# Performance work log

Hardware: AMD Instinct MI355X
Metric: run time of the kernel (lower is better)

Reference implementation:

```python
import jax, jax.numpy as jnp
import numpy as np

B, LC, LE, H, V = 128, 256, 257, 512, 128
PAD = 0  # padding_token_index


def lstm_cell(x, h, c, Wih, Whh, b):
    # torch LSTMCell gate order: i, f, g, o
    g = x @ Wih.T + h @ Whh.T + b
    i, f, gg, o = jnp.split(g, 4, axis=-1)
    c = jax.nn.sigmoid(f) * c + jax.nn.sigmoid(i) * jnp.tanh(gg)
    h = jax.nn.sigmoid(o) * jnp.tanh(c)
    return h, c


def setup_inputs() -> dict:
    key = jax.random.key(0)
    ks = jax.random.split(key, 32)
    p = lambda k, shape: jax.random.normal(k, shape, jnp.float32) * 0.05
    d = {
        'C_idx': jax.random.randint(ks[0], (B, LC), 0, V, dtype=jnp.int32),
        'E_idx': jax.random.randint(ks[1], (B, LE), 0, V, dtype=jnp.int32),
        'C_pad': jnp.zeros((B, LC), dtype=bool),
        'enc_Wih_f': p(ks[2], (4 * H, V)),
        'enc_Whh_f': p(ks[3], (4 * H, H)),
        'enc_b_f': p(ks[4], (4 * H,)),
        'enc_Wih_b': p(ks[5], (4 * H, V)),
        'enc_Whh_b': p(ks[6], (4 * H, H)),
        'enc_b_b': p(ks[7], (4 * H,)),
        'dec_Wih': p(ks[8], (4 * H, H + V)),
        'dec_Whh': p(ks[9], (4 * H, H)),
        'dec_b': p(ks[10], (4 * H,)),
        'Wh': p(ks[11], (H, 2 * H)),
        'Wc': p(ks[12], (H, 2 * H)),
        'Wattn': p(ks[13], (H, 2 * H)),
        'Wout': p(ks[14], (H, 3 * H)),
        'Wvocab': p(ks[15], (V, H)),
        'pg_ctx': p(ks[16], (2 * H,)),
        'pg_in': p(ks[17], (V + H,)),
        'pg_h': p(ks[18], (H,)),
        'pg_c': p(ks[19], (H,)),
        'pg_b': p(ks[20], (1,)),
    }
    return d


def _forward(C_idx, E_idx, C_pad, enc_Wih_f, enc_Whh_f, enc_b_f, enc_Wih_b, enc_Whh_b, enc_b_b,
             dec_Wih, dec_Whh, dec_b, Wh, Wc, Wattn, Wout, Wvocab,
             pg_ctx, pg_in, pg_h, pg_c, pg_b):
    C = jax.nn.one_hot(C_idx, V, dtype=jnp.float32)      # [B,LC,V]
    E_emb = jax.nn.one_hot(E_idx, V, dtype=jnp.float32)  # [B,LE,V]
    z = jnp.zeros((B, H), jnp.float32)

    xs = jnp.swapaxes(C, 0, 1)  # [LC,B,V]

    def enc_fwd(carry, x):
        h, c = lstm_cell(x, carry[0], carry[1], enc_Wih_f, enc_Whh_f, enc_b_f)
        return (h, c), h

    def enc_bwd(carry, x):
        h, c = lstm_cell(x, carry[0], carry[1], enc_Wih_b, enc_Whh_b, enc_b_b)
        return (h, c), h

    (hf, cf), Hf = jax.lax.scan(enc_fwd, (z, z), xs)
    (hb, cb), Hb = jax.lax.scan(enc_bwd, (z, z), xs[::-1])
    Hb = Hb[::-1]
    enc = jnp.swapaxes(jnp.concatenate([Hf, Hb], axis=-1), 0, 1)  # [B,LC,2H]

    # decoder init state from final encoder states (fwd;bwd concat)
    h0 = jnp.concatenate([hf, hb], axis=-1) @ Wh.T
    c0 = jnp.concatenate([cf, cb], axis=-1) @ Wc.T

    enc_proj = enc @ Wattn.T  # [B,LC,H]

    def step(carry, x_emb):
        h, c, prev_out = carry
        nin = jnp.concatenate([x_emb, prev_out], axis=1)  # [B,V+H]
        h, c = lstm_cell(nin, h, c, dec_Wih, dec_Whh, dec_b)
        scores = jnp.einsum('blh,bh->bl', enc_proj, h)
        scores = jnp.where(C_pad, -jnp.inf, scores)
        attn = jax.nn.softmax(scores, axis=1)             # [B,LC]
        ctx = jnp.einsum('bl,blh->bh', attn, enc)         # [B,2H]
        t_out = jnp.tanh(jnp.concatenate([h, ctx], axis=1) @ Wout.T)  # [B,H]
        gen = jax.nn.softmax(t_out @ Wvocab.T, axis=1)    # [B,V]
        p_gen = jax.nn.sigmoid(ctx @ pg_ctx + nin @ pg_in + h @ pg_h + c @ pg_c + pg_b[0])[:, None]
        copy_p = attn * (1.0 - p_gen)
        out = jax.vmap(lambda o, idx, a: o.at[idx].add(a))(gen * p_gen, C_idx, copy_p)
        return (h, c, t_out), out

    xs2 = jnp.swapaxes(E_emb[:, :LE - 1], 0, 1)  # teacher inputs, step 0 = start token
    _, preds = jax.lax.scan(step, (h0, c0, z), xs2)
    preds = jnp.swapaxes(preds, 0, 1)  # [B,LE-1,V]

    tgt = E_idx[:, 1:]
    nll = -jnp.take_along_axis(jnp.log(preds), tgt[..., None], axis=2)[..., 0]
    return jnp.where(tgt == PAD, 0.0, nll)  # [B,LE-1], reduction='none'


def reference(C_idx, E_idx, C_pad, enc_Wih_f, enc_Whh_f, enc_b_f, enc_Wih_b, enc_Whh_b, enc_b_b,
              dec_Wih, dec_Whh, dec_b, Wh, Wc, Wattn, Wout, Wvocab,
              pg_ctx, pg_in, pg_h, pg_c, pg_b):
    return _forward(C_idx, E_idx, C_pad, enc_Wih_f, enc_Whh_f, enc_b_f, enc_Wih_b, enc_Whh_b, enc_b_b,
                    dec_Wih, dec_Whh, dec_b, Wh, Wc, Wattn, Wout, Wvocab,
                    pg_ctx, pg_in, pg_h, pg_c, pg_b)
```

## Files before the change

### kernel.cpp

```cpp
#include <hip/hip_runtime.h>

static constexpr int B_   = 128;
static constexpr int LC_  = 256;
static constexpr int LE_  = 257;
static constexpr int H_   = 512;
static constexpr size_t HB_ = (size_t)512 * 128;

static constexpr size_t OFF_ENC    = 0;
static constexpr size_t SZ_ENC     = (size_t)128 * 256 * 1024 * 2;
static constexpr size_t OFF_WIHFT  = OFF_ENC + SZ_ENC;
static constexpr size_t OFF_WIHBT  = OFF_WIHFT + (size_t)128 * 2048 * 4;
static constexpr size_t OFF_XDEC   = OFF_WIHBT + (size_t)128 * 2048 * 4;
static constexpr size_t OFF_WATTNT = OFF_XDEC + (size_t)128 * 2048 * 4;
static constexpr size_t OFF_HENC   = OFF_WATTNT + (size_t)1024 * 512 * 4;
static constexpr size_t OFF_CENC   = OFF_HENC + 4 * HB_ * 4;
static constexpr size_t OFF_HDEC   = OFF_CENC + 2 * HB_ * 4;
static constexpr size_t OFF_CDEC   = OFF_HDEC + 2 * HB_ * 4;
static constexpr size_t OFF_TOUT   = OFF_CDEC + HB_ * 4;
static constexpr size_t OFF_U      = OFF_TOUT + 2 * HB_ * 4;
static constexpr size_t OFF_CTX    = OFF_U + (size_t)1024 * 128 * 4;
static constexpr size_t OFF_SC     = OFF_CTX + (size_t)1024 * 128 * 4;
static constexpr size_t OFF_MD     = OFF_SC + (size_t)128 * 256 * 4;

__device__ __forceinline__ float sigm(float x) { return 1.f / (1.f + expf(-x)); }
__device__ __forceinline__ unsigned short f2bf(float f) {
  unsigned u = __float_as_uint(f);
  u += 0x7fffu + ((u >> 16) & 1u);
  return (unsigned short)(u >> 16);
}
__device__ __forceinline__ float bfl(unsigned w) { return __uint_as_float(w << 16); }
__device__ __forceinline__ float bfh(unsigned w) { return __uint_as_float(w & 0xffff0000u); }

__global__ __launch_bounds__(256) void k_pre(const float* __restrict__ wihF,
                                             const float* __restrict__ wihB,
                                             const float* __restrict__ dWih,
                                             const float* __restrict__ Wattn,
                                             float* __restrict__ ws) {
  float* WT_F = (float*)((char*)ws + OFF_WIHFT);
  float* WT_B = (float*)((char*)ws + OFF_WIHBT);
  float* XD   = (float*)((char*)ws + OFF_XDEC);
  float* WAT  = (float*)((char*)ws + OFF_WATTNT);
  int stride = gridDim.x * blockDim.x;
  int i0 = blockIdx.x * blockDim.x + threadIdx.x;
  for (int x = i0; x < 128 * 2048; x += stride) {
    int v = x >> 11, n = x & 2047;
    WT_F[x] = wihF[n * 128 + v];
    WT_B[x] = wihB[n * 128 + v];
    XD[x]   = dWih[n * 640 + v];
  }
  for (int x = i0; x < 1024 * 512; x += stride) {
    int j = x >> 9, i2 = x & 511;
    WAT[x] = Wattn[i2 * 1024 + j];
  }
}

__global__ __launch_bounds__(512) void k_enc(const float* __restrict__ WhhF,
                                             const float* __restrict__ WhhB,
                                             const float* __restrict__ bF,
                                             const float* __restrict__ bB,
                                             const int* __restrict__ C_idx,
                                             float* __restrict__ ws, int t) {
  int p = blockIdx.x * 512 + threadIdx.x;
  int b = p & 127;
  int j = (p >> 7) & 511;
  int dir = p >> 16;
  int jj = __builtin_amdgcn_readfirstlane(j);
  int dd = __builtin_amdgcn_readfirstlane(dir);
  const float* Whh  = dd ? WhhB : WhhF;
  const float* bias = dd ? bB : bF;
  const float* WihT = (const float*)((char*)ws + (dd ? OFF_WIHBT : OFF_WIHFT));
  int l = dd ? (LC_ - 1 - t) : t;
  int cidx = C_idx[b * LC_ + l];
  int par = t & 1;
  const float* hp = (const float*)((char*)ws + OFF_HENC) + (size_t)(dir * 2 + (par ^ 1)) * HB_ + b;

  const float* w0 = Whh + (size_t)jj * 512;
  const float* w1 = Whh + (size_t)(512 + jj) * 512;
  const float* w2 = Whh + (size_t)(1024 + jj) * 512;
  const float* w3 = Whh + (size_t)(1536 + jj) * 512;
  float a0 = bias[jj]        + WihT[(size_t)cidx * 2048 + jj];
  float a1 = bias[512 + jj]  + WihT[(size_t)cidx * 2048 + 512 + jj];
  float a2 = bias[1024 + jj] + WihT[(size_t)cidx * 2048 + 1024 + jj];
  float a3 = bias[1536 + jj] + WihT[(size_t)cidx * 2048 + 1536 + jj];
  for (int k = 0; k < 512; k += 4) {
    float4 W0 = *(const float4*)(w0 + k);
    float4 W1 = *(const float4*)(w1 + k);
    float4 W2 = *(const float4*)(w2 + k);
    float4 W3 = *(const float4*)(w3 + k);
    float h0 = hp[(size_t)k * 128], h1 = hp[(size_t)(k + 1) * 128];
    float h2 = hp[(size_t)(k + 2) * 128], h3 = hp[(size_t)(k + 3) * 128];
    a0 += W0.x * h0 + W0.y * h1 + W0.z * h2 + W0.w * h3;
    a1 += W1.x * h0 + W1.y * h1 + W1.z * h2 + W1.w * h3;
    a2 += W2.x * h0 + W2.y * h1 + W2.z * h2 + W2.w * h3;
    a3 += W3.x * h0 + W3.y * h1 + W3.z * h2 + W3.w * h3;
  }
  float ig = sigm(a0), fg = sigm(a1), gg = tanhf(a2), og = sigm(a3);
  float* cp = (float*)((char*)ws + OFF_CENC) + (size_t)dir * HB_ + (size_t)j * 128 + b;
  float c = fg * (*cp) + ig * gg;
  *cp = c;
  float h = og * tanhf(c);
  ((float*)((char*)ws + OFF_HENC))[(size_t)(dir * 2 + par) * HB_ + (size_t)j * 128 + b] = h;
  ((unsigned short*)((char*)ws + OFF_ENC))[((size_t)b * LC_ + l) * 1024 + dir * 512 + j] = f2bf(h);
}

__global__ __launch_bounds__(512) void k_h0c0(const float* __restrict__ Wh,
                                              const float* __restrict__ Wc,
                                              float* __restrict__ ws) {
  int p = blockIdx.x * 512 + threadIdx.x;
  int b = p & 127;
  int n = (p >> 7) & 511;
  int sel = p >> 16;
  int nn = __builtin_amdgcn_readfirstlane(n);
  int ss = __builtin_amdgcn_readfirstlane(sel);
  const float* W = (ss ? Wc : Wh) + (size_t)nn * 1024;
  const float* hf = (const float*)((char*)ws + OFF_HENC) + (size_t)1 * HB_ + b;
  const float* hb = (const float*)((char*)ws + OFF_HENC) + (size_t)3 * HB_ + b;
  float acc = 0.f;
  for (int k = 0; k < 512; k += 4) {
    float4 Wa = *(const float4*)(W + k);
    float4 Wb = *(const float4*)(W + 512 + k);
    acc += Wa.x * hf[(size_t)k * 128] + Wa.y * hf[(size_t)(k + 1) * 128]
         + Wa.z * hf[(size_t)(k + 2) * 128] + Wa.w * hf[(size_t)(k + 3) * 128];
    acc += Wb.x * hb[(size_t)k * 128] + Wb.y * hb[(size_t)(k + 1) * 128]
         + Wb.z * hb[(size_t)(k + 2) * 128] + Wb.w * hb[(size_t)(k + 3) * 128];
  }
  float* dst = (float*)((char*)ws + (ss ? OFF_CDEC : OFF_HDEC));
  dst[(size_t)n * 128 + b] = acc;
}

__device__ void s4_body(float* __restrict__ ws, float* __restrict__ out,
                        const float* __restrict__ Wvocab, const int* __restrict__ E_idx,
                        const int* __restrict__ C_idx, int b, int t) {
  __shared__ float to[516];
  __shared__ float lgp[128][4];
  __shared__ float lg[128];
  __shared__ float red2[8];
  __shared__ float mx_s[2];
  int tau = threadIdx.x;
  const float* TO = (const float*)((char*)ws + OFF_TOUT) + (size_t)(t & 1) * HB_;
  to[tau + (tau >> 7)] = TO[(size_t)tau * 128 + b];
  __syncthreads();
  int v = tau >> 2, seg = tau & 3;
  const float* wv = Wvocab + (size_t)v * 512 + seg * 128;
  const float* tp = &to[seg * 128 + seg];
  float part = 0.f;
#pragma unroll 8
  for (int i = 0; i < 128; ++i) part += tp[i] * wv[i];
  lgp[v][seg] = part;
  __syncthreads();
  if (tau < 128) lg[tau] = lgp[tau][0] + lgp[tau][1] + lgp[tau][2] + lgp[tau][3];
  __syncthreads();
  if (tau < 64) {
    float m2 = fmaxf(lg[tau], lg[tau + 64]);
    for (int o = 32; o; o >>= 1) m2 = fmaxf(m2, __shfl_xor(m2, o));
    float e = expf(lg[tau] - m2) + expf(lg[tau + 64] - m2);
    for (int o = 32; o; o >>= 1) e += __shfl_xor(e, o);
    if (tau == 0) { mx_s[0] = m2; mx_s[1] = e; }
  }
  const float* MD = (const float*)((char*)ws + OFF_MD);
  float Mb = MD[b], Db = MD[128 + b], pg = MD[256 + b];
  int tgt = E_idx[b * LE_ + t];
  float cm = 0.f;
  if (tau < 256) {
    float s = ((const float*)((char*)ws + OFF_SC))[b * 256 + tau];
    if (C_idx[b * 256 + tau] == tgt) cm = expf(s - Mb);
  }
  for (int o = 32; o; o >>= 1) cm += __shfl_xor(cm, o);
  if ((tau & 63) == 0) red2[tau >> 6] = cm;
  __syncthreads();
  if (tau == 0) {
    float mass = (red2[0] + red2[1] + red2[2] + red2[3]) / Db;
    float gen_tgt = expf(lg[tgt] - mx_s[0]) / mx_s[1];
    float prob = pg * gen_tgt + (1.f - pg) * mass;
    out[b * 256 + (t - 1)] = (tgt == 0) ? 0.f : -logf(prob);
  }
}

__global__ __launch_bounds__(512) void k_dgates(const float* __restrict__ dWih,
                                                const float* __restrict__ dWhh,
                                                const float* __restrict__ db,
                                                const float* __restrict__ Wvocab,
                                                const int* __restrict__ E_idx,
                                                const int* __restrict__ C_idx,
                                                float* __restrict__ ws,
                                                float* __restrict__ out, int t) {
  int tau = threadIdx.x;
  if (blockIdx.x >= 256) {
    if (t > 0) s4_body(ws, out, Wvocab, E_idx, C_idx, blockIdx.x - 256, t);
    return;
  }
  __shared__ float part[4][256];
  int kh = tau >> 8, q = tau & 255;
  int pp = blockIdx.x * 256 + q;
  int b = pp & 127, j = pp >> 7;
  int jj = __builtin_amdgcn_readfirstlane(j);
  int pr = t & 1;
  float a0 = 0.f, a1 = 0.f, a2 = 0.f, a3 = 0.f;
  if (kh == 0) {
    const float* w0 = dWih + (size_t)jj * 640 + 128;
    const float* w1 = dWih + (size_t)(512 + jj) * 640 + 128;
    const float* w2 = dWih + (size_t)(1024 + jj) * 640 + 128;
    const float* w3 = dWih + (size_t)(1536 + jj) * 640 + 128;
    const float* po = (const float*)((char*)ws + OFF_TOUT) + (size_t)pr * HB_ + b;
    for (int k = 0; k < 512; k += 4) {
      float4 W0 = *(const float4*)(w0 + k);
      float4 W1 = *(const float4*)(w1 + k);
      float4 W2 = *(const float4*)(w2 + k);
      float4 W3 = *(const float4*)(w3 + k);
      float h0 = po[(size_t)k * 128], h1 = po[(size_t)(k + 1) * 128];
      float h2 = po[(size_t)(k + 2) * 128], h3 = po[(size_t)(k + 3) * 128];
      a0 += W0.x * h0 + W0.y * h1 + W0.z * h2 + W0.w * h3;
      a1 += W1.x * h0 + W1.y * h1 + W1.z * h2 + W1.w * h3;
      a2 += W2.x * h0 + W2.y * h1 + W2.z * h2 + W2.w * h3;
      a3 += W3.x * h0 + W3.y * h1 + W3.z * h2 + W3.w * h3;
    }
  } else {
    const float* w0 = dWhh + (size_t)jj * 512;
    const float* w1 = dWhh + (size_t)(512 + jj) * 512;
    const float* w2 = dWhh + (size_t)(1024 + jj) * 512;
    const float* w3 = dWhh + (size_t)(1536 + jj) * 512;
    const float* hp = (const float*)((char*)ws + OFF_HDEC) + (size_t)pr * HB_ + b;
    for (int k = 0; k < 512; k += 4) {
      float4 W0 = *(const float4*)(w0 + k);
      float4 W1 = *(const float4*)(w1 + k);
      float4 W2 = *(const float4*)(w2 + k);
      float4 W3 = *(const float4*)(w3 + k);
      float h0 = hp[(size_t)k * 128], h1 = hp[(size_t)(k + 1) * 128];
      float h2 = hp[(size_t)(k + 2) * 128], h3 = hp[(size_t)(k + 3) * 128];
      a0 += W0.x * h0 + W0.y * h1 + W0.z * h2 + W0.w * h3;
      a1 += W1.x * h0 + W1.y * h1 + W1.z * h2 + W1.w * h3;
      a2 += W2.x * h0 + W2.y * h1 + W2.z * h2 + W2.w * h3;
      a3 += W3.x * h0 + W3.y * h1 + W3.z * h2 + W3.w * h3;
    }
    part[0][q] = a0; part[1][q] = a1; part[2][q] = a2; part[3][q] = a3;
  }
  __syncthreads();
  if (kh == 0) {
    int xid = E_idx[b * LE_ + t];
    const float* xg = (const float*)((char*)ws + OFF_XDEC) + (size_t)xid * 2048;
    float g0 = a0 + part[0][q] + db[jj]        + xg[jj];
    float g1 = a1 + part[1][q] + db[512 + jj]  + xg[512 + jj];
    float g2 = a2 + part[2][q] + db[1024 + jj] + xg[1024 + jj];
    float g3 = a3 + part[3][q] + db[1536 + jj] + xg[1536 + jj];
    float ig = sigm(g0), fg = sigm(g1), gg = tanhf(g2), og = sigm(g3);
    float* cp = (float*)((char*)ws + OFF_CDEC) + (size_t)j * 128 + b;
    float c = fg * (*cp) + ig * gg;
    *cp = c;
    ((float*)((char*)ws + OFF_HDEC))[(size_t)(pr ^ 1) * HB_ + (size_t)j * 128 + b] = og * tanhf(c);
  }
}

__global__ __launch_bounds__(512) void k_u(const float* __restrict__ unused,
                                           float* __restrict__ ws, int t) {
  int p = blockIdx.x * 512 + threadIdx.x;
  int b = p & 127, j = p >> 7;
  int jj = __builtin_amdgcn_readfirstlane(j);
  const float* w = (const float*)((char*)ws + OFF_WATTNT) + (size_t)jj * 512;
  const float* hp = (const float*)((char*)ws + OFF_HDEC) + (size_t)((t & 1) ^ 1) * HB_ + b;
  float acc = 0.f;
  for (int k = 0; k < 512; k += 4) {
    float4 W = *(const float4*)(w + k);
    acc += W.x * hp[(size_t)k * 128] + W.y * hp[(size_t)(k + 1) * 128]
         + W.z * hp[(size_t)(k + 2) * 128] + W.w * hp[(size_t)(k + 3) * 128];
  }
  ((float*)((char*)ws + OFF_U))[(size_t)j * 128 + b] = acc;
}

__global__ __launch_bounds__(512) void k_attn(const float* __restrict__ pg_ctx,
                                              const float* __restrict__ pg_in,
                                              const float* __restrict__ pg_h,
                                              const float* __restrict__ pg_c,
                                              const float* __restrict__ pg_b,
                                              const int* __restrict__ E_idx,
                                              const unsigned char* __restrict__ C_pad,
                                              float* __restrict__ ws, int t) {
  __shared__ unsigned short tile[65536];
  __shared__ float u_lds[1032];
  __shared__ float scp[64][9];
  __shared__ float p_lds[64];
  __shared__ float sred[8];
  __shared__ float bc[2];
  int b = blockIdx.x, tau = threadIdx.x;
  int pr = t & 1;
  const float* U = (const float*)((char*)ws + OFF_U);
  u_lds[tau + (tau >> 7)] = U[(size_t)tau * 128 + b];
  {
    int x2 = tau + 512;
    u_lds[x2 + (x2 >> 7)] = U[(size_t)x2 * 128 + b];
  }
  float M = -3.0e38f, D = 0.f, c0 = 0.f, c1 = 0.f;
  const uint4* encb = (const uint4*)((char*)ws + OFF_ENC + (size_t)b * LC_ * 1024 * 2);
  float* SC = (float*)((char*)ws + OFF_SC);
  int l = tau >> 3, seg = tau & 7;
  for (int lb = 0; lb < 4; ++lb) {
    const uint4* src = encb + (size_t)lb * 64 * 128;
#pragma unroll
    for (int it = 0; it < 16; ++it) {
      int fl = it * 512 + tau;
      int r = fl >> 7, cb = fl & 127;
      ((uint4*)tile)[(r << 7) + (cb ^ (r & 7))] = src[fl];
    }
    __syncthreads();
    float acc = 0.f;
#pragma unroll
    for (int ibv = 0; ibv < 16; ++ibv) {
      int blk = (seg * 16 + ibv) ^ (l & 7);
      const uint4 wv = *(const uint4*)&tile[(l << 10) + (blk << 3)];
      const float* up = &u_lds[seg * 128 + ibv * 8 + seg];
      acc += bfl(wv.x) * up[0] + bfh(wv.x) * up[1];
      acc += bfl(wv.y) * up[2] + bfh(wv.y) * up[3];
      acc += bfl(wv.z) * up[4] + bfh(wv.z) * up[5];
      acc += bfl(wv.w) * up[6] + bfh(wv.w) * up[7];
    }
    scp[l][seg] = acc;
    __syncthreads();
    if (tau < 64) {
      float s = scp[tau][0] + scp[tau][1] + scp[tau][2] + scp[tau][3]
              + scp[tau][4] + scp[tau][5] + scp[tau][6] + scp[tau][7];
      int gl = lb * 64 + tau;
      if (C_pad[b * LC_ + gl]) s = -3.0e38f;
      SC[b * 256 + gl] = s;
      float m = s;
      for (int o = 32; o; o >>= 1) m = fmaxf(m, __shfl_xor(m, o));
      float Mn = fmaxf(M, m);
      float pv = expf(s - Mn);
      p_lds[tau] = pv;
      float ds = pv;
      for (int o = 32; o; o >>= 1) ds += __shfl_xor(ds, o);
      if (tau == 0) { bc[0] = m; bc[1] = ds; }
    }
    __syncthreads();
    float Mn = fmaxf(M, bc[0]);
    float scale = expf(M - Mn);
    D = D * scale + bc[1];
    c0 *= scale; c1 *= scale;
    M = Mn;
    {
      int cb0 = tau >> 3, e0 = tau & 7;
      int cb1 = (tau + 512) >> 3;
#pragma unroll 8
      for (int l2 = 0; l2 < 64; ++l2) {
        float pv = p_lds[l2];
        float v0 = bfl((unsigned)tile[(l2 << 10) + (((cb0 ^ (l2 & 7)) << 3) | e0)]);
        float v1 = bfl((unsigned)tile[(l2 << 10) + (((cb1 ^ (l2 & 7)) << 3) | e0)]);
        c0 += pv * v0; c1 += pv * v1;
      }
    }
    __syncthreads();
  }
  float inv = 1.f / D;
  float x0 = c0 * inv, x1 = c1 * inv;
  float* CTX = (float*)((char*)ws + OFF_CTX);
  CTX[(size_t)tau * 128 + b] = x0;
  CTX[(size_t)(tau + 512) * 128 + b] = x1;
  float pp = x0 * pg_ctx[tau] + x1 * pg_ctx[tau + 512];
  pp += ((const float*)((char*)ws + OFF_HDEC))[(size_t)(pr ^ 1) * HB_ + (size_t)tau * 128 + b] * pg_h[tau];
  pp += ((const float*)((char*)ws + OFF_CDEC))[(size_t)tau * 128 + b] * pg_c[tau];
  pp += ((const float*)((char*)ws + OFF_TOUT))[(size_t)pr * HB_ + (size_t)tau * 128 + b] * pg_in[128 + tau];
  for (int o = 32; o; o >>= 1) pp += __shfl_xor(pp, o);
  if ((tau & 63) == 0) sred[tau >> 6] = pp;
  __syncthreads();
  if (tau == 0) {
    float s = sred[0] + sred[1] + sred[2] + sred[3] + sred[4] + sred[5] + sred[6] + sred[7];
    int xid = E_idx[b * LE_ + t];
    s += pg_in[xid] + pg_b[0];
    float* MD = (float*)((char*)ws + OFF_MD);
    MD[256 + b] = sigm(s);
    MD[b] = M;
    MD[128 + b] = D;
  }
}

__global__ __launch_bounds__(512) void k_wout(const float* __restrict__ Wout,
                                              float* __restrict__ ws, int t) {
  __shared__ float part[256];
  int tau = threadIdx.x;
  int kh = tau >> 8, q = tau & 255;
  int pp = blockIdx.x * 256 + q;
  int b = pp & 127, n = pp >> 7;
  int nn = __builtin_amdgcn_readfirstlane(n);
  int pr = t & 1;
  float acc = 0.f;
  if (kh == 0) {
    const float* w = Wout + (size_t)nn * 1536;
    const float* hp = (const float*)((char*)ws + OFF_HDEC) + (size_t)(pr ^ 1) * HB_ + b;
    for (int k = 0; k < 512; k += 4) {
      float4 W = *(const float4*)(w + k);
      acc += W.x * hp[(size_t)k * 128] + W.y * hp[(size_t)(k + 1) * 128]
           + W.z * hp[(size_t)(k + 2) * 128] + W.w * hp[(size_t)(k + 3) * 128];
    }
  } else {
    const float* w = Wout + (size_t)nn * 1536 + 512;
    const float* cp = (const float*)((char*)ws + OFF_CTX) + b;
    for (int k = 0; k < 1024; k += 4) {
      float4 W = *(const float4*)(w + k);
      acc += W.x * cp[(size_t)k * 128] + W.y * cp[(size_t)(k + 1) * 128]
           + W.z * cp[(size_t)(k + 2) * 128] + W.w * cp[(size_t)(k + 3) * 128];
    }
    part[q] = acc;
  }
  __syncthreads();
  if (kh == 0) {
    float s = acc + part[q];
    ((float*)((char*)ws + OFF_TOUT))[(size_t)(pr ^ 1) * HB_ + (size_t)n * 128 + b] = tanhf(s);
  }
}

__global__ __launch_bounds__(512) void k_final(const float* __restrict__ Wvocab,
                                               const int* __restrict__ E_idx,
                                               const int* __restrict__ C_idx,
                                               float* __restrict__ ws,
                                               float* __restrict__ out) {
  s4_body(ws, out, Wvocab, E_idx, C_idx, blockIdx.x, 256);
}

extern "C" void kernel_launch(void* const* d_in, const int* in_sizes, int n_in,
                              void* d_out, int out_size, void* d_ws, size_t ws_size,
                              hipStream_t stream) {
  (void)in_sizes; (void)n_in; (void)out_size; (void)ws_size;
  const int* C_idx = (const int*)d_in[0];
  const int* E_idx = (const int*)d_in[1];
  const unsigned char* C_pad = (const unsigned char*)d_in[2];
  const float* eWihF = (const float*)d_in[3];
  const float* eWhhF = (const float*)d_in[4];
  const float* ebF   = (const float*)d_in[5];
  const float* eWihB = (const float*)d_in[6];
  const float* eWhhB = (const float*)d_in[7];
  const float* ebB   = (const float*)d_in[8];
  const float* dWih  = (const float*)d_in[9];
  const float* dWhh  = (const float*)d_in[10];
  const float* db    = (const float*)d_in[11];
  const float* Wh    = (const float*)d_in[12];
  const float* Wc    = (const float*)d_in[13];
  const float* Wattn = (const float*)d_in[14];
  const float* Wout  = (const float*)d_in[15];
  const float* Wvoc  = (const float*)d_in[16];
  const float* pgc   = (const float*)d_in[17];
  const float* pgi   = (const float*)d_in[18];
  const float* pgh   = (const float*)d_in[19];
  const float* pgcc  = (const float*)d_in[20];
  const float* pgb   = (const float*)d_in[21];
  float* ws = (float*)d_ws;
  float* out = (float*)d_out;

  hipMemsetAsync((char*)d_ws + OFF_HENC, 0, 6 * HB_ * 4, stream);
  hipMemsetAsync((char*)d_ws + OFF_TOUT, 0, 2 * HB_ * 4, stream);

  k_pre<<<512, 256, 0, stream>>>(eWihF, eWihB, dWih, Wattn, ws);
  for (int t = 0; t < 256; ++t)
    k_enc<<<256, 512, 0, stream>>>(eWhhF, eWhhB, ebF, ebB, C_idx, ws, t);
  k_h0c0<<<256, 512, 0, stream>>>(Wh, Wc, ws);
  for (int t = 0; t < 256; ++t) {
    k_dgates<<<384, 512, 0, stream>>>(dWih, dWhh, db, Wvoc, E_idx, C_idx, ws, out, t);
    k_u<<<256, 512, 0, stream>>>(nullptr, ws, t);
    k_attn<<<128, 512, 0, stream>>>(pgc, pgi, pgh, pgcc, pgb, E_idx, C_pad, ws, t);
    k_wout<<<256, 512, 0, stream>>>(Wout, ws, t);
  }
  k_final<<<128, 512, 0, stream>>>(Wvoc, E_idx, C_idx, ws, out);
}
```

Measured before the change: 34.11 ms.

## Replace per-timestep kernel launches with persistent per-batch encoder and decoder kernels

```diff
diff --git a/kernel.cpp b/kernel.cpp
--- a/kernel.cpp
+++ b/kernel.cpp
@@ -1,26 +1,9 @@
 #include <hip/hip_runtime.h>
 
-static constexpr int B_   = 128;
-static constexpr int LC_  = 256;
-static constexpr int LE_  = 257;
-static constexpr int H_   = 512;
-static constexpr size_t HB_ = (size_t)512 * 128;
-
-static constexpr size_t OFF_ENC    = 0;
-static constexpr size_t SZ_ENC     = (size_t)128 * 256 * 1024 * 2;
-static constexpr size_t OFF_WIHFT  = OFF_ENC + SZ_ENC;
-static constexpr size_t OFF_WIHBT  = OFF_WIHFT + (size_t)128 * 2048 * 4;
-static constexpr size_t OFF_XDEC   = OFF_WIHBT + (size_t)128 * 2048 * 4;
-static constexpr size_t OFF_WATTNT = OFF_XDEC + (size_t)128 * 2048 * 4;
-static constexpr size_t OFF_HENC   = OFF_WATTNT + (size_t)1024 * 512 * 4;
-static constexpr size_t OFF_CENC   = OFF_HENC + 4 * HB_ * 4;
-static constexpr size_t OFF_HDEC   = OFF_CENC + 2 * HB_ * 4;
-static constexpr size_t OFF_CDEC   = OFF_HDEC + 2 * HB_ * 4;
-static constexpr size_t OFF_TOUT   = OFF_CDEC + HB_ * 4;
-static constexpr size_t OFF_U      = OFF_TOUT + 2 * HB_ * 4;
-static constexpr size_t OFF_CTX    = OFF_U + (size_t)1024 * 128 * 4;
-static constexpr size_t OFF_SC     = OFF_CTX + (size_t)1024 * 128 * 4;
-static constexpr size_t OFF_MD     = OFF_SC + (size_t)128 * 256 * 4;
+static constexpr size_t OFF_ENC  = 0;
+static constexpr size_t OFF_HFIN = 67108864;
+static constexpr size_t OFF_CFIN = 67633152;
+static constexpr size_t OFF_OVL  = 68157440;
 
 __device__ __forceinline__ float sigm(float x) { return 1.f / (1.f + expf(-x)); }
 __device__ __forceinline__ unsigned short f2bf(float f) {
@@ -30,388 +13,391 @@
 }
 __device__ __forceinline__ float bfl(unsigned w) { return __uint_as_float(w << 16); }
 __device__ __forceinline__ float bfh(unsigned w) { return __uint_as_float(w & 0xffff0000u); }
-
-__global__ __launch_bounds__(256) void k_pre(const float* __restrict__ wihF,
-                                             const float* __restrict__ wihB,
-                                             const float* __restrict__ dWih,
-                                             const float* __restrict__ Wattn,
-                                             float* __restrict__ ws) {
-  float* WT_F = (float*)((char*)ws + OFF_WIHFT);
-  float* WT_B = (float*)((char*)ws + OFF_WIHBT);
-  float* XD   = (float*)((char*)ws + OFF_XDEC);
-  float* WAT  = (float*)((char*)ws + OFF_WATTNT);
-  int stride = gridDim.x * blockDim.x;
-  int i0 = blockIdx.x * blockDim.x + threadIdx.x;
-  for (int x = i0; x < 128 * 2048; x += stride) {
-    int v = x >> 11, n = x & 2047;
-    WT_F[x] = wihF[n * 128 + v];
-    WT_B[x] = wihB[n * 128 + v];
-    XD[x]   = dWih[n * 640 + v];
-  }
-  for (int x = i0; x < 1024 * 512; x += stride) {
-    int j = x >> 9, i2 = x & 511;
-    WAT[x] = Wattn[i2 * 1024 + j];
-  }
-}
-
-__global__ __launch_bounds__(512) void k_enc(const float* __restrict__ WhhF,
-                                             const float* __restrict__ WhhB,
-                                             const float* __restrict__ bF,
+__device__ __forceinline__ float bf2f(unsigned short v) { return __uint_as_float(((unsigned)v) << 16); }
+
+#if defined(__has_builtin)
+#if __has_builtin(__builtin_amdgcn_fdot2_f32_bf16)
+#define HAVE_DOT2BF 1
+#endif
+#endif
+
+#ifdef HAVE_DOT2BF
+typedef __bf16 bf2_t __attribute__((ext_vector_type(2)));
+__device__ __forceinline__ float dot2bf(unsigned w, unsigned h, float acc) {
+  return __builtin_amdgcn_fdot2_f32_bf16(__builtin_bit_cast(bf2_t, w),
+                                         __builtin_bit_cast(bf2_t, h), acc, false);
+}
+#else
+__device__ __forceinline__ float dot2bf(unsigned w, unsigned h, float acc) {
+  return acc + bfl(w) * bfl(h) + bfh(w) * bfh(h);
+}
+#endif
+
+__global__ __launch_bounds__(256) void k_pre1(const float* __restrict__ WhhF,
+                                              const float* __restrict__ WhhB,
+                                              const float* __restrict__ WihF,
+                                              const float* __restrict__ WihB,
+                                              char* __restrict__ wsb) {
+  unsigned short* dst = (unsigned short*)(wsb + OFF_OVL);
+  int id = blockIdx.x * 256 + threadIdx.x;
+  int str = gridDim.x * 256;
+  for (int x = id; x < 2097152; x += str) {
+    int dir = x >> 20, r = x & 1048575;
+    int e = r & 7, j = (r >> 3) & 511, k2 = r >> 12;
+    int g = e >> 1, k = k2 * 2 + (e & 1);
+    const float* W = dir ? WhhB : WhhF;
+    dst[x] = f2bf(W[((size_t)g * 512 + j) * 512 + k]);
+  }
+  for (int x = id; x < 524288; x += str) {
+    int dir = x >> 18, r = x & 262143;
+    int g = r & 3, j = (r >> 2) & 511, v = r >> 11;
+    const float* W = dir ? WihB : WihF;
+    dst[2097152 + x] = f2bf(W[((size_t)g * 512 + j) * 128 + v]);
+  }
+}
+
+__global__ __launch_bounds__(256) void k_pre2(const float* __restrict__ dWih,
+                                              const float* __restrict__ dWhh,
+                                              const float* __restrict__ Wattn,
+                                              const float* __restrict__ Wout,
+                                              const float* __restrict__ Wvoc,
+                                              char* __restrict__ wsb) {
+  unsigned short* dst = (unsigned short*)(wsb + OFF_OVL);
+  int id = blockIdx.x * 256 + threadIdx.x;
+  int str = gridDim.x * 256;
+  for (int x = id; x < 1048576; x += str) {
+    int e = x & 7, j = (x >> 3) & 511, k2 = x >> 12;
+    int g = e >> 1, k = k2 * 2 + (e & 1);
+    dst[x] = f2bf(dWih[((size_t)g * 512 + j) * 640 + 128 + k]);
+  }
+  for (int x = id; x < 1048576; x += str) {
+    int e = x & 7, j = (x >> 3) & 511, k2 = x >> 12;
+    int g = e >> 1, k = k2 * 2 + (e & 1);
+    dst[1048576 + x] = f2bf(dWhh[((size_t)g * 512 + j) * 512 + k]);
+  }
+  for (int x = id; x < 524288; x += str) {
+    int e = x & 3, o = (x >> 2) & 1023, i4 = x >> 12;
+    int i = i4 * 4 + e;
+    dst[2097152 + x] = f2bf(Wattn[(size_t)i * 1024 + o]);
+  }
+  for (int x = id; x < 786432; x += str) {
+    int e = x & 3, j = (x >> 2) & 511, i4 = x >> 11;
+    int i = i4 * 4 + e;
+    dst[2621440 + x] = f2bf(Wout[(size_t)j * 1536 + i]);
+  }
+  for (int x = id; x < 65536; x += str) {
+    int e = x & 3, v = (x >> 2) & 127, i4 = x >> 9;
+    int i = i4 * 4 + e;
+    dst[3407872 + x] = f2bf(Wvoc[(size_t)v * 512 + i]);
+  }
+  for (int x = id; x < 262144; x += str) {
+    int g = x & 3, j = (x >> 2) & 511, v = x >> 11;
+    dst[3473408 + x] = f2bf(dWih[((size_t)g * 512 + j) * 640 + v]);
+  }
+}
+
+__global__ __launch_bounds__(512) void k_enc(const float* __restrict__ bF,
                                              const float* __restrict__ bB,
                                              const int* __restrict__ C_idx,
-                                             float* __restrict__ ws, int t) {
-  int p = blockIdx.x * 512 + threadIdx.x;
-  int b = p & 127;
-  int j = (p >> 7) & 511;
-  int dir = p >> 16;
-  int jj = __builtin_amdgcn_readfirstlane(j);
-  int dd = __builtin_amdgcn_readfirstlane(dir);
-  const float* Whh  = dd ? WhhB : WhhF;
-  const float* bias = dd ? bB : bF;
-  const float* WihT = (const float*)((char*)ws + (dd ? OFF_WIHBT : OFF_WIHFT));
-  int l = dd ? (LC_ - 1 - t) : t;
-  int cidx = C_idx[b * LC_ + l];
-  int par = t & 1;
-  const float* hp = (const float*)((char*)ws + OFF_HENC) + (size_t)(dir * 2 + (par ^ 1)) * HB_ + b;
-
-  const float* w0 = Whh + (size_t)jj * 512;
-  const float* w1 = Whh + (size_t)(512 + jj) * 512;
-  const float* w2 = Whh + (size_t)(1024 + jj) * 512;
-  const float* w3 = Whh + (size_t)(1536 + jj) * 512;
-  float a0 = bias[jj]        + WihT[(size_t)cidx * 2048 + jj];
-  float a1 = bias[512 + jj]  + WihT[(size_t)cidx * 2048 + 512 + jj];
-  float a2 = bias[1024 + jj] + WihT[(size_t)cidx * 2048 + 1024 + jj];
-  float a3 = bias[1536 + jj] + WihT[(size_t)cidx * 2048 + 1536 + jj];
-  for (int k = 0; k < 512; k += 4) {
-    float4 W0 = *(const float4*)(w0 + k);
-    float4 W1 = *(const float4*)(w1 + k);
-    float4 W2 = *(const float4*)(w2 + k);
-    float4 W3 = *(const float4*)(w3 + k);
-    float h0 = hp[(size_t)k * 128], h1 = hp[(size_t)(k + 1) * 128];
-    float h2 = hp[(size_t)(k + 2) * 128], h3 = hp[(size_t)(k + 3) * 128];
-    a0 += W0.x * h0 + W0.y * h1 + W0.z * h2 + W0.w * h3;
-    a1 += W1.x * h0 + W1.y * h1 + W1.z * h2 + W1.w * h3;
-    a2 += W2.x * h0 + W2.y * h1 + W2.z * h2 + W2.w * h3;
-    a3 += W3.x * h0 + W3.y * h1 + W3.z * h2 + W3.w * h3;
-  }
-  float ig = sigm(a0), fg = sigm(a1), gg = tanhf(a2), og = sigm(a3);
-  float* cp = (float*)((char*)ws + OFF_CENC) + (size_t)dir * HB_ + (size_t)j * 128 + b;
-  float c = fg * (*cp) + ig * gg;
-  *cp = c;
-  float h = og * tanhf(c);
-  ((float*)((char*)ws + OFF_HENC))[(size_t)(dir * 2 + par) * HB_ + (size_t)j * 128 + b] = h;
-  ((unsigned short*)((char*)ws + OFF_ENC))[((size_t)b * LC_ + l) * 1024 + dir * 512 + j] = f2bf(h);
-}
-
-__global__ __launch_bounds__(512) void k_h0c0(const float* __restrict__ Wh,
-                                              const float* __restrict__ Wc,
-                                              float* __restrict__ ws) {
-  int p = blockIdx.x * 512 + threadIdx.x;
-  int b = p & 127;
-  int n = (p >> 7) & 511;
-  int sel = p >> 16;
-  int nn = __builtin_amdgcn_readfirstlane(n);
-  int ss = __builtin_amdgcn_readfirstlane(sel);
-  const float* W = (ss ? Wc : Wh) + (size_t)nn * 1024;
-  const float* hf = (const float*)((char*)ws + OFF_HENC) + (size_t)1 * HB_ + b;
-  const float* hb = (const float*)((char*)ws + OFF_HENC) + (size_t)3 * HB_ + b;
-  float acc = 0.f;
-  for (int k = 0; k < 512; k += 4) {
-    float4 Wa = *(const float4*)(W + k);
-    float4 Wb = *(const float4*)(W + 512 + k);
-    acc += Wa.x * hf[(size_t)k * 128] + Wa.y * hf[(size_t)(k + 1) * 128]
-         + Wa.z * hf[(size_t)(k + 2) * 128] + Wa.w * hf[(size_t)(k + 3) * 128];
-    acc += Wb.x * hb[(size_t)k * 128] + Wb.y * hb[(size_t)(k + 1) * 128]
-         + Wb.z * hb[(size_t)(k + 2) * 128] + Wb.w * hb[(size_t)(k + 3) * 128];
-  }
-  float* dst = (float*)((char*)ws + (ss ? OFF_CDEC : OFF_HDEC));
-  dst[(size_t)n * 128 + b] = acc;
-}
-
-__device__ void s4_body(float* __restrict__ ws, float* __restrict__ out,
-                        const float* __restrict__ Wvocab, const int* __restrict__ E_idx,
-                        const int* __restrict__ C_idx, int b, int t) {
-  __shared__ float to[516];
-  __shared__ float lgp[128][4];
-  __shared__ float lg[128];
-  __shared__ float red2[8];
-  __shared__ float mx_s[2];
+                                             char* __restrict__ wsb) {
+  __shared__ __align__(16) unsigned short hbf[512];
+  int bid = blockIdx.x;
+  int b = bid & 127, dir = bid >> 7;
+  int j = threadIdx.x;
+  const unsigned short* WH = (const unsigned short*)(wsb + OFF_OVL) + (size_t)dir * 1048576;
+  const unsigned short* WX = (const unsigned short*)(wsb + OFF_OVL) + 2097152 + (size_t)dir * 262144;
+  const float* bias = dir ? bB : bF;
+  float b0 = bias[j], b1 = bias[512 + j], b2 = bias[1024 + j], b3 = bias[1536 + j];
+  unsigned short* encb = (unsigned short*)wsb + (size_t)b * 262144;
+  const uint4* wp = (const uint4*)WH + j;
+  float c = 0.f, h = 0.f;
+  hbf[j] = 0;
+  __syncthreads();
+  for (int t = 0; t < 256; ++t) {
+    int l = dir ? (255 - t) : t;
+    int cidx = C_idx[b * 256 + l];
+    uint2 xg = *(const uint2*)(WX + ((size_t)cidx * 512 + j) * 4);
+    float a0 = b0 + bfl(xg.x), a1 = b1 + bfh(xg.x);
+    float a2 = b2 + bfl(xg.y), a3 = b3 + bfh(xg.y);
+    for (int k2 = 0; k2 < 256; ++k2) {
+      uint4 w = wp[(size_t)k2 * 512];
+      unsigned hp = *(const unsigned*)((const char*)hbf + k2 * 4);
+      a0 = dot2bf(w.x, hp, a0);
+      a1 = dot2bf(w.y, hp, a1);
+      a2 = dot2bf(w.z, hp, a2);
+      a3 = dot2bf(w.w, hp, a3);
+    }
+    float ig = sigm(a0), fg = sigm(a1), gg = tanhf(a2), og = sigm(a3);
+    c = fg * c + ig * gg;
+    h = og * tanhf(c);
+    __syncthreads();
+    unsigned short hb = f2bf(h);
+    hbf[j] = hb;
+    encb[(size_t)l * 1024 + dir * 512 + j] = hb;
+    __syncthreads();
+  }
+  ((float*)(wsb + OFF_HFIN))[((size_t)b * 2 + dir) * 512 + j] = h;
+  ((float*)(wsb + OFF_CFIN))[((size_t)b * 2 + dir) * 512 + j] = c;
+}
+
+__global__ __launch_bounds__(1024, 4) void k_dec(
+    const int* __restrict__ C_idx, const int* __restrict__ E_idx,
+    const unsigned char* __restrict__ C_pad,
+    const float* __restrict__ db, const float* __restrict__ Wh, const float* __restrict__ Wc,
+    const float* __restrict__ pgc, const float* __restrict__ pgi,
+    const float* __restrict__ pgh, const float* __restrict__ pgcc, const float* __restrict__ pgb,
+    char* __restrict__ wsb, float* __restrict__ out) {
+  __shared__ __align__(16) unsigned short inbf[1536];
+  __shared__ __align__(16) unsigned short tobf[512];
+  __shared__ __align__(16) unsigned short ubf[1024];
+  __shared__ float cst[512];
+  __shared__ float hf32[512];
+  __shared__ float ctxf[1024];
+  __shared__ __align__(16) float part[2][512][4];
+  __shared__ float sc[256];
+  __shared__ float pr[256];
+  __shared__ float red[16];
+  __shared__ float scal[4];
+  __shared__ float lgf[128];
+
+  int b = blockIdx.x;
   int tau = threadIdx.x;
-  const float* TO = (const float*)((char*)ws + OFF_TOUT) + (size_t)(t & 1) * HB_;
-  to[tau + (tau >> 7)] = TO[(size_t)tau * 128 + b];
-  __syncthreads();
-  int v = tau >> 2, seg = tau & 3;
-  const float* wv = Wvocab + (size_t)v * 512 + seg * 128;
-  const float* tp = &to[seg * 128 + seg];
-  float part = 0.f;
-#pragma unroll 8
-  for (int i = 0; i < 128; ++i) part += tp[i] * wv[i];
-  lgp[v][seg] = part;
-  __syncthreads();
-  if (tau < 128) lg[tau] = lgp[tau][0] + lgp[tau][1] + lgp[tau][2] + lgp[tau][3];
-  __syncthreads();
-  if (tau < 64) {
-    float m2 = fmaxf(lg[tau], lg[tau + 64]);
-    for (int o = 32; o; o >>= 1) m2 = fmaxf(m2, __shfl_xor(m2, o));
-    float e = expf(lg[tau] - m2) + expf(lg[tau + 64] - m2);
-    for (int o = 32; o; o >>= 1) e += __shfl_xor(e, o);
-    if (tau == 0) { mx_s[0] = m2; mx_s[1] = e; }
-  }
-  const float* MD = (const float*)((char*)ws + OFF_MD);
-  float Mb = MD[b], Db = MD[128 + b], pg = MD[256 + b];
-  int tgt = E_idx[b * LE_ + t];
-  float cm = 0.f;
-  if (tau < 256) {
-    float s = ((const float*)((char*)ws + OFF_SC))[b * 256 + tau];
-    if (C_idx[b * 256 + tau] == tgt) cm = expf(s - Mb);
-  }
-  for (int o = 32; o; o >>= 1) cm += __shfl_xor(cm, o);
-  if ((tau & 63) == 0) red2[tau >> 6] = cm;
-  __syncthreads();
-  if (tau == 0) {
-    float mass = (red2[0] + red2[1] + red2[2] + red2[3]) / Db;
-    float gen_tgt = expf(lg[tgt] - mx_s[0]) / mx_s[1];
-    float prob = pg * gen_tgt + (1.f - pg) * mass;
-    out[b * 256 + (t - 1)] = (tgt == 0) ? 0.f : -logf(prob);
-  }
-}
-
-__global__ __launch_bounds__(512) void k_dgates(const float* __restrict__ dWih,
-                                                const float* __restrict__ dWhh,
-                                                const float* __restrict__ db,
-                                                const float* __restrict__ Wvocab,
-                                                const int* __restrict__ E_idx,
-                                                const int* __restrict__ C_idx,
-                                                float* __restrict__ ws,
-                                                float* __restrict__ out, int t) {
-  int tau = threadIdx.x;
-  if (blockIdx.x >= 256) {
-    if (t > 0) s4_body(ws, out, Wvocab, E_idx, C_idx, blockIdx.x - 256, t);
-    return;
-  }
-  __shared__ float part[4][256];
-  int kh = tau >> 8, q = tau & 255;
-  int pp = blockIdx.x * 256 + q;
-  int b = pp & 127, j = pp >> 7;
-  int jj = __builtin_amdgcn_readfirstlane(j);
-  int pr = t & 1;
-  float a0 = 0.f, a1 = 0.f, a2 = 0.f, a3 = 0.f;
-  if (kh == 0) {
-    const float* w0 = dWih + (size_t)jj * 640 + 128;
-    const float* w1 = dWih + (size_t)(512 + jj) * 640 + 128;
-    const float* w2 = dWih + (size_t)(1024 + jj) * 640 + 128;
-    const float* w3 = dWih + (size_t)(1536 + jj) * 640 + 128;
-    const float* po = (const float*)((char*)ws + OFF_TOUT) + (size_t)pr * HB_ + b;
-    for (int k = 0; k < 512; k += 4) {
-      float4 W0 = *(const float4*)(w0 + k);
-      float4 W1 = *(const float4*)(w1 + k);
-      float4 W2 = *(const float4*)(w2 + k);
-      float4 W3 = *(const float4*)(w3 + k);
-      float h0 = po[(size_t)k * 128], h1 = po[(size_t)(k + 1) * 128];
-      float h2 = po[(size_t)(k + 2) * 128], h3 = po[(size_t)(k + 3) * 128];
-      a0 += W0.x * h0 + W0.y * h1 + W0.z * h2 + W0.w * h3;
-      a1 += W1.x * h0 + W1.y * h1 + W1.z * h2 + W1.w * h3;
-      a2 += W2.x * h0 + W2.y * h1 + W2.z * h2 + W2.w * h3;
-      a3 += W3.x * h0 + W3.y * h1 + W3.z * h2 + W3.w * h3;
-    }
-  } else {
-    const float* w0 = dWhh + (size_t)jj * 512;
-    const float* w1 = dWhh + (size_t)(512 + jj) * 512;
-    const float* w2 = dWhh + (size_t)(1024 + jj) * 512;
-    const float* w3 = dWhh + (size_t)(1536 + jj) * 512;
-    const float* hp = (const float*)((char*)ws + OFF_HDEC) + (size_t)pr * HB_ + b;
-    for (int k = 0; k < 512; k += 4) {
-      float4 W0 = *(const float4*)(w0 + k);
-      float4 W1 = *(const float4*)(w1 + k);
-      float4 W2 = *(const float4*)(w2 + k);
-      float4 W3 = *(const float4*)(w3 + k);
-      float h0 = hp[(size_t)k * 128], h1 = hp[(size_t)(k + 1) * 128];
-      float h2 = hp[(size_t)(k + 2) * 128], h3 = hp[(size_t)(k + 3) * 128];
-      a0 += W0.x * h0 + W0.y * h1 + W0.z * h2 + W0.w * h3;
-      a1 += W1.x * h0 + W1.y * h1 + W1.z * h2 + W1.w * h3;
-      a2 += W2.x * h0 + W2.y * h1 + W2.z * h2 + W2.w * h3;
-      a3 += W3.x * h0 + W3.y * h1 + W3.z * h2 + W3.w * h3;
-    }
-    part[0][q] = a0; part[1][q] = a1; part[2][q] = a2; part[3][q] = a3;
-  }
-  __syncthreads();
-  if (kh == 0) {
-    int xid = E_idx[b * LE_ + t];
-    const float* xg = (const float*)((char*)ws + OFF_XDEC) + (size_t)xid * 2048;
-    float g0 = a0 + part[0][q] + db[jj]        + xg[jj];
-    float g1 = a1 + part[1][q] + db[512 + jj]  + xg[512 + jj];
-    float g2 = a2 + part[2][q] + db[1024 + jj] + xg[1024 + jj];
-    float g3 = a3 + part[3][q] + db[1536 + jj] + xg[1536 + jj];
-    float ig = sigm(g0), fg = sigm(g1), gg = tanhf(g2), og = sigm(g3);
-    float* cp = (float*)((char*)ws + OFF_CDEC) + (size_t)j * 128 + b;
-    float c = fg * (*cp) + ig * gg;
-    *cp = c;
-    ((float*)((char*)ws + OFF_HDEC))[(size_t)(pr ^ 1) * HB_ + (size_t)j * 128 + b] = og * tanhf(c);
-  }
-}
-
-__global__ __launch_bounds__(512) void k_u(const float* __restrict__ unused,
-                                           float* __restrict__ ws, int t) {
-  int p = blockIdx.x * 512 + threadIdx.x;
-  int b = p & 127, j = p >> 7;
-  int jj = __builtin_amdgcn_readfirstlane(j);
-  const float* w = (const float*)((char*)ws + OFF_WATTNT) + (size_t)jj * 512;
-  const float* hp = (const float*)((char*)ws + OFF_HDEC) + (size_t)((t & 1) ^ 1) * HB_ + b;
-  float acc = 0.f;
-  for (int k = 0; k < 512; k += 4) {
-    float4 W = *(const float4*)(w + k);
-    acc += W.x * hp[(size_t)k * 128] + W.y * hp[(size_t)(k + 1) * 128]
-         + W.z * hp[(size_t)(k + 2) * 128] + W.w * hp[(size_t)(k + 3) * 128];
-  }
-  ((float*)((char*)ws + OFF_U))[(size_t)j * 128 + b] = acc;
-}
-
-__global__ __launch_bounds__(512) void k_attn(const float* __restrict__ pg_ctx,
-                                              const float* __restrict__ pg_in,
-                                              const float* __restrict__ pg_h,
-                                              const float* __restrict__ pg_c,
-                                              const float* __restrict__ pg_b,
-                                              const int* __restrict__ E_idx,
-                                              const unsigned char* __restrict__ C_pad,
-                                              float* __restrict__ ws, int t) {
-  __shared__ unsigned short tile[65536];
-  __shared__ float u_lds[1032];
-  __shared__ float scp[64][9];
-  __shared__ float p_lds[64];
-  __shared__ float sred[8];
-  __shared__ float bc[2];
-  int b = blockIdx.x, tau = threadIdx.x;
-  int pr = t & 1;
-  const float* U = (const float*)((char*)ws + OFF_U);
-  u_lds[tau + (tau >> 7)] = U[(size_t)tau * 128 + b];
+  int lane = tau & 63;
+  int wv = tau >> 6;
+
+  const unsigned short* DWIH = (const unsigned short*)(wsb + OFF_OVL);
+  const unsigned short* DWHH = DWIH + 1048576;
+  const unsigned short* WATT = DWIH + 2097152;
+  const unsigned short* WOUT = DWIH + 2621440;
+  const unsigned short* WVOC = DWIH + 3407872;
+  const unsigned short* XDEC = DWIH + 3473408;
+  const unsigned short* encB = (const unsigned short*)wsb + (size_t)b * 262144;
+
   {
-    int x2 = tau + 512;
-    u_lds[x2 + (x2 >> 7)] = U[(size_t)x2 * 128 + b];
-  }
-  float M = -3.0e38f, D = 0.f, c0 = 0.f, c1 = 0.f;
-  const uint4* encb = (const uint4*)((char*)ws + OFF_ENC + (size_t)b * LC_ * 1024 * 2);
-  float* SC = (float*)((char*)ws + OFF_SC);
-  int l = tau >> 3, seg = tau & 7;
-  for (int lb = 0; lb < 4; ++lb) {
-    const uint4* src = encb + (size_t)lb * 64 * 128;
-#pragma unroll
-    for (int it = 0; it < 16; ++it) {
-      int fl = it * 512 + tau;
-      int r = fl >> 7, cb = fl & 127;
-      ((uint4*)tile)[(r << 7) + (cb ^ (r & 7))] = src[fl];
-    }
-    __syncthreads();
-    float acc = 0.f;
-#pragma unroll
-    for (int ibv = 0; ibv < 16; ++ibv) {
-      int blk = (seg * 16 + ibv) ^ (l & 7);
-      const uint4 wv = *(const uint4*)&tile[(l << 10) + (blk << 3)];
-      const float* up = &u_lds[seg * 128 + ibv * 8 + seg];
-      acc += bfl(wv.x) * up[0] + bfh(wv.x) * up[1];
-      acc += bfl(wv.y) * up[2] + bfh(wv.y) * up[3];
-      acc += bfl(wv.z) * up[4] + bfh(wv.z) * up[5];
-      acc += bfl(wv.w) * up[6] + bfh(wv.w) * up[7];
-    }
-    scp[l][seg] = acc;
-    __syncthreads();
-    if (tau < 64) {
-      float s = scp[tau][0] + scp[tau][1] + scp[tau][2] + scp[tau][3]
-              + scp[tau][4] + scp[tau][5] + scp[tau][6] + scp[tau][7];
-      int gl = lb * 64 + tau;
-      if (C_pad[b * LC_ + gl]) s = -3.0e38f;
-      SC[b * 256 + gl] = s;
+    float* catH = &part[0][0][0];
+    float* catC = catH + 1024;
+    const float* HF = (const float*)(wsb + OFF_HFIN) + (size_t)b * 1024;
+    const float* CF = (const float*)(wsb + OFF_CFIN) + (size_t)b * 1024;
+    if (tau < 1024) { catH[tau] = HF[tau]; catC[tau] = CF[tau]; }
+    __syncthreads();
+    for (int oo = 0; oo < 64; ++oo) {
+      int o = wv * 64 + oo;
+      int sel = o >> 9, j = o & 511;
+      const float* Wrow = (sel ? Wc : Wh) + (size_t)j * 1024;
+      const float* inp = sel ? catC : catH;
+      float a = 0.f;
+      for (int p = 0; p < 4; ++p) {
+        float4 wf = *(const float4*)(Wrow + p * 256 + lane * 4);
+        float4 iv = *(const float4*)(inp + p * 256 + lane * 4);
+        a += wf.x * iv.x + wf.y * iv.y + wf.z * iv.z + wf.w * iv.w;
+      }
+      for (int o2 = 32; o2; o2 >>= 1) a += __shfl_xor(a, o2);
+      if (lane == 0) {
+        if (sel == 0) { hf32[j] = a; inbf[j] = f2bf(a); }
+        else cst[j] = a;
+      }
+    }
+    if (tau < 512) tobf[tau] = 0;
+    __syncthreads();
+  }
+
+  for (int t = 0; t < 256; ++t) {
+    int xid = E_idx[b * 257 + t];
+    int tgt = E_idx[b * 257 + t + 1];
+
+    {
+      int half = tau >> 9, j = tau & 511;
+      const unsigned short* W = half ? DWHH : DWIH;
+      const unsigned short* inb = half ? (const unsigned short*)inbf
+                                       : (const unsigned short*)tobf;
+      const uint4* wp = (const uint4*)W + j;
+      float a0 = 0.f, a1 = 0.f, a2 = 0.f, a3 = 0.f;
+      for (int k2 = 0; k2 < 256; ++k2) {
+        uint4 w = wp[(size_t)k2 * 512];
+        unsigned hp = *(const unsigned*)((const char*)inb + k2 * 4);
+        a0 = dot2bf(w.x, hp, a0);
+        a1 = dot2bf(w.y, hp, a1);
+        a2 = dot2bf(w.z, hp, a2);
+        a3 = dot2bf(w.w, hp, a3);
+      }
+      *(float4*)&part[half][j][0] = make_float4(a0, a1, a2, a3);
+    }
+    __syncthreads();
+    if (tau < 512) {
+      int j = tau;
+      float4 p0 = *(const float4*)&part[0][j][0];
+      float4 p1 = *(const float4*)&part[1][j][0];
+      uint2 xg = *(const uint2*)(XDEC + ((size_t)xid * 512 + j) * 4);
+      float g0 = p0.x + p1.x + db[j] + bfl(xg.x);
+      float g1 = p0.y + p1.y + db[512 + j] + bfh(xg.x);
+      float g2 = p0.z + p1.z + db[1024 + j] + bfl(xg.y);
+      float g3 = p0.w + p1.w + db[1536 + j] + bfh(xg.y);
+      float ig = sigm(g0), fg = sigm(g1), gg = tanhf(g2), og = sigm(g3);
+      float c = fg * cst[j] + ig * gg;
+      cst[j] = c;
+      float h = og * tanhf(c);
+      hf32[j] = h;
+      inbf[j] = f2bf(h);
+    }
+    __syncthreads();
+    {
+      const uint2* wp = (const uint2*)WATT + tau;
+      float au = 0.f;
+      for (int i4 = 0; i4 < 128; ++i4) {
+        uint2 w = wp[(size_t)i4 * 1024];
+        uint2 hp = *(const uint2*)((const char*)inbf + i4 * 8);
+        au = dot2bf(w.x, hp.x, au);
+        au = dot2bf(w.y, hp.y, au);
+      }
+      ubf[tau] = f2bf(au);
+    }
+    __syncthreads();
+    {
+      uint4 u0 = *(const uint4*)((const char*)ubf + lane * 16);
+      uint4 u1 = *(const uint4*)((const char*)ubf + 1024 + lane * 16);
+      for (int li = 0; li < 16; ++li) {
+        int l = wv * 16 + li;
+        const uint4* e0 = (const uint4*)(encB + (size_t)l * 1024) + lane;
+        uint4 ea = e0[0];
+        uint4 eb = e0[64];
+        float s = 0.f;
+        s = dot2bf(ea.x, u0.x, s); s = dot2bf(ea.y, u0.y, s);
+        s = dot2bf(ea.z, u0.z, s); s = dot2bf(ea.w, u0.w, s);
+        s = dot2bf(eb.x, u1.x, s); s = dot2bf(eb.y, u1.y, s);
+        s = dot2bf(eb.z, u1.z, s); s = dot2bf(eb.w, u1.w, s);
+        for (int o2 = 32; o2; o2 >>= 1) s += __shfl_xor(s, o2);
+        if (lane == 0) sc[l] = s;
+      }
+    }
+    __syncthreads();
+    if (tau < 256) {
+      float s = sc[tau];
+      if (C_pad[b * 256 + tau]) s = -3.0e38f;
+      sc[tau] = s;
       float m = s;
-      for (int o = 32; o; o >>= 1) m = fmaxf(m, __shfl_xor(m, o));
-      float Mn = fmaxf(M, m);
-      float pv = expf(s - Mn);
-      p_lds[tau] = pv;
-      float ds = pv;
-      for (int o = 32; o; o >>= 1) ds += __shfl_xor(ds, o);
-      if (tau == 0) { bc[0] = m; bc[1] = ds; }
-    }
-    __syncthreads();
-    float Mn = fmaxf(M, bc[0]);
-    float scale = expf(M - Mn);
-    D = D * scale + bc[1];
-    c0 *= scale; c1 *= scale;
-    M = Mn;
-    {
-      int cb0 = tau >> 3, e0 = tau & 7;
-      int cb1 = (tau + 512) >> 3;
-#pragma unroll 8
-      for (int l2 = 0; l2 < 64; ++l2) {
-        float pv = p_lds[l2];
-        float v0 = bfl((unsigned)tile[(l2 << 10) + (((cb0 ^ (l2 & 7)) << 3) | e0)]);
-        float v1 = bfl((unsigned)tile[(l2 << 10) + (((cb1 ^ (l2 & 7)) << 3) | e0)]);
-        c0 += pv * v0; c1 += pv * v1;
-      }
-    }
-    __syncthreads();
-  }
-  float inv = 1.f / D;
-  float x0 = c0 * inv, x1 = c1 * inv;
-  float* CTX = (float*)((char*)ws + OFF_CTX);
-  CTX[(size_t)tau * 128 + b] = x0;
-  CTX[(size_t)(tau + 512) * 128 + b] = x1;
-  float pp = x0 * pg_ctx[tau] + x1 * pg_ctx[tau + 512];
-  pp += ((const float*)((char*)ws + OFF_HDEC))[(size_t)(pr ^ 1) * HB_ + (size_t)tau * 128 + b] * pg_h[tau];
-  pp += ((const float*)((char*)ws + OFF_CDEC))[(size_t)tau * 128 + b] * pg_c[tau];
-  pp += ((const float*)((char*)ws + OFF_TOUT))[(size_t)pr * HB_ + (size_t)tau * 128 + b] * pg_in[128 + tau];
-  for (int o = 32; o; o >>= 1) pp += __shfl_xor(pp, o);
-  if ((tau & 63) == 0) sred[tau >> 6] = pp;
-  __syncthreads();
-  if (tau == 0) {
-    float s = sred[0] + sred[1] + sred[2] + sred[3] + sred[4] + sred[5] + sred[6] + sred[7];
-    int xid = E_idx[b * LE_ + t];
-    s += pg_in[xid] + pg_b[0];
-    float* MD = (float*)((char*)ws + OFF_MD);
-    MD[256 + b] = sigm(s);
-    MD[b] = M;
-    MD[128 + b] = D;
-  }
-}
-
-__global__ __launch_bounds__(512) void k_wout(const float* __restrict__ Wout,
-                                              float* __restrict__ ws, int t) {
-  __shared__ float part[256];
-  int tau = threadIdx.x;
-  int kh = tau >> 8, q = tau & 255;
-  int pp = blockIdx.x * 256 + q;
-  int b = pp & 127, n = pp >> 7;
-  int nn = __builtin_amdgcn_readfirstlane(n);
-  int pr = t & 1;
-  float acc = 0.f;
-  if (kh == 0) {
-    const float* w = Wout + (size_t)nn * 1536;
-    const float* hp = (const float*)((char*)ws + OFF_HDEC) + (size_t)(pr ^ 1) * HB_ + b;
-    for (int k = 0; k < 512; k += 4) {
-      float4 W = *(const float4*)(w + k);
-      acc += W.x * hp[(size_t)k * 128] + W.y * hp[(size_t)(k + 1) * 128]
-           + W.z * hp[(size_t)(k + 2) * 128] + W.w * hp[(size_t)(k + 3) * 128];
-    }
-  } else {
-    const float* w = Wout + (size_t)nn * 1536 + 512;
-    const float* cp = (const float*)((char*)ws + OFF_CTX) + b;
-    for (int k = 0; k < 1024; k += 4) {
-      float4 W = *(const float4*)(w + k);
-      acc += W.x * cp[(size_t)k * 128] + W.y * cp[(size_t)(k + 1) * 128]
-           + W.z * cp[(size_t)(k + 2) * 128] + W.w * cp[(size_t)(k + 3) * 128];
-    }
-    part[q] = acc;
-  }
-  __syncthreads();
-  if (kh == 0) {
-    float s = acc + part[q];
-    ((float*)((char*)ws + OFF_TOUT))[(size_t)(pr ^ 1) * HB_ + (size_t)n * 128 + b] = tanhf(s);
-  }
-}
-
-__global__ __launch_bounds__(512) void k_final(const float* __restrict__ Wvocab,
-                                               const int* __restrict__ E_idx,
-                                               const int* __restrict__ C_idx,
-                                               float* __restrict__ ws,
-                                               float* __restrict__ out) {
-  s4_body(ws, out, Wvocab, E_idx, C_idx, blockIdx.x, 256);
+      for (int o2 = 32; o2; o2 >>= 1) m = fmaxf(m, __shfl_xor(m, o2));
+      if (lane == 0) red[wv] = m;
+    }
+    __syncthreads();
+    if (tau < 256) {
+      float M = fmaxf(fmaxf(red[0], red[1]), fmaxf(red[2], red[3]));
+      float e = expf(sc[tau] - M);
+      pr[tau] = e;
+      float sum = e;
+      for (int o2 = 32; o2; o2 >>= 1) sum += __shfl_xor(sum, o2);
+      if (lane == 0) red[4 + wv] = sum;
+    }
+    __syncthreads();
+    if (tau < 256) {
+      float D = red[4] + red[5] + red[6] + red[7];
+      pr[tau] = pr[tau] / D;
+    }
+    __syncthreads();
+    if (tau < 512) {
+      const unsigned short* ep = encB + tau * 2;
+      float ax = 0.f, ay = 0.f;
+      for (int l = 0; l < 256; ++l) {
+        unsigned w = *(const unsigned*)(ep + (size_t)l * 1024);
+        float p = pr[l];
+        ax += p * bfl(w);
+        ay += p * bfh(w);
+      }
+      ctxf[2 * tau] = ax;
+      ctxf[2 * tau + 1] = ay;
+      unsigned packed = (unsigned)f2bf(ax) | ((unsigned)f2bf(ay) << 16);
+      *(unsigned*)&inbf[512 + 2 * tau] = packed;
+    }
+    __syncthreads();
+    {
+      float acc = 0.f;
+      if (tau < 512) {
+        int j = tau;
+        acc = hf32[j] * pgh[j] + cst[j] * pgcc[j] + bf2f(tobf[j]) * pgi[128 + j]
+            + ctxf[j] * pgc[j] + ctxf[512 + j] * pgc[512 + j];
+      }
+      for (int o2 = 32; o2; o2 >>= 1) acc += __shfl_xor(acc, o2);
+      if (lane == 0) red[wv] = acc;
+    }
+    __syncthreads();
+    if (tau == 0) {
+      float s = 0.f;
+      for (int i = 0; i < 8; ++i) s += red[i];
+      s += pgi[xid] + pgb[0];
+      scal[0] = sigm(s);
+    }
+    __syncthreads();
+    {
+      int half = tau >> 9, j = tau & 511;
+      const uint2* wp = (const uint2*)WOUT + j;
+      float a = 0.f;
+      int i40 = half * 192;
+      for (int i4 = 0; i4 < 192; ++i4) {
+        uint2 w = wp[(size_t)(i40 + i4) * 512];
+        uint2 ip = *(const uint2*)((const char*)inbf + (i40 + i4) * 8);
+        a = dot2bf(w.x, ip.x, a);
+        a = dot2bf(w.y, ip.y, a);
+      }
+      part[0][j][half] = a;
+    }
+    __syncthreads();
+    if (tau < 512) {
+      float tv = tanhf(part[0][tau][0] + part[0][tau][1]);
+      tobf[tau] = f2bf(tv);
+    }
+    __syncthreads();
+    {
+      float* lgp = &part[0][0][0];
+      int v = tau >> 3, seg = tau & 7;
+      const uint2* wp = (const uint2*)WVOC + v;
+      float a = 0.f;
+      for (int i4i = 0; i4i < 16; ++i4i) {
+        int i4 = seg * 16 + i4i;
+        uint2 w = wp[(size_t)i4 * 128];
+        uint2 ip = *(const uint2*)((const char*)tobf + i4 * 8);
+        a = dot2bf(w.x, ip.x, a);
+        a = dot2bf(w.y, ip.y, a);
+      }
+      lgp[v * 8 + seg] = a;
+    }
+    __syncthreads();
+    {
+      float* lgp = &part[0][0][0];
+      if (tau < 128) {
+        float lg = 0.f;
+        for (int s8 = 0; s8 < 8; ++s8) lg += lgp[tau * 8 + s8];
+        lgf[tau] = lg;
+        float m = lg;
+        for (int o2 = 32; o2; o2 >>= 1) m = fmaxf(m, __shfl_xor(m, o2));
+        if (lane == 0) red[8 + wv] = m;
+      }
+    }
+    __syncthreads();
+    if (tau < 128) {
+      float mx = fmaxf(red[8], red[9]);
+      float e = expf(lgf[tau] - mx);
+      for (int o2 = 32; o2; o2 >>= 1) e += __shfl_xor(e, o2);
+      if (lane == 0) red[10 + wv] = e;
+      if (tau == 0) red[12] = mx;
+    }
+    __syncthreads();
+    {
+      float cm = 0.f;
+      if (tau < 256 && C_idx[b * 256 + tau] == tgt) cm = pr[tau];
+      for (int o2 = 32; o2; o2 >>= 1) cm += __shfl_xor(cm, o2);
+      if (lane == 0 && wv < 4) red[wv] = cm;
+    }
+    __syncthreads();
+    if (tau == 0) {
+      float Pg = scal[0];
+      float mx = red[12];
+      float sume = red[10] + red[11];
+      float gen_tgt = expf(lgf[tgt] - mx) / sume;
+      float copy = (red[0] + red[1] + red[2] + red[3]) * (1.f - Pg);
+      float prob = Pg * gen_tgt + copy;
+      out[b * 256 + t] = (tgt == 0) ? 0.f : -logf(prob);
+    }
+    __syncthreads();
+  }
 }
 
 extern "C" void kernel_launch(void* const* d_in, const int* in_sizes, int n_in,
@@ -440,21 +426,12 @@
   const float* pgh   = (const float*)d_in[19];
   const float* pgcc  = (const float*)d_in[20];
   const float* pgb   = (const float*)d_in[21];
-  float* ws = (float*)d_ws;
+  char* wsb = (char*)d_ws;
   float* out = (float*)d_out;
 
-  hipMemsetAsync((char*)d_ws + OFF_HENC, 0, 6 * HB_ * 4, stream);
-  hipMemsetAsync((char*)d_ws + OFF_TOUT, 0, 2 * HB_ * 4, stream);
-
-  k_pre<<<512, 256, 0, stream>>>(eWihF, eWihB, dWih, Wattn, ws);
-  for (int t = 0; t < 256; ++t)
-    k_enc<<<256, 512, 0, stream>>>(eWhhF, eWhhB, ebF, ebB, C_idx, ws, t);
-  k_h0c0<<<256, 512, 0, stream>>>(Wh, Wc, ws);
-  for (int t = 0; t < 256; ++t) {
-    k_dgates<<<384, 512, 0, stream>>>(dWih, dWhh, db, Wvoc, E_idx, C_idx, ws, out, t);
-    k_u<<<256, 512, 0, stream>>>(nullptr, ws, t);
-    k_attn<<<128, 512, 0, stream>>>(pgc, pgi, pgh, pgcc, pgb, E_idx, C_pad, ws, t);
-    k_wout<<<256, 512, 0, stream>>>(Wout, ws, t);
-  }
-  k_final<<<128, 512, 0, stream>>>(Wvoc, E_idx, C_idx, ws, out);
-}
+  k_pre1<<<256, 256, 0, stream>>>(eWhhF, eWhhB, eWihF, eWihB, wsb);
+  k_enc<<<256, 512, 0, stream>>>(ebF, ebB, C_idx, wsb);
+  k_pre2<<<256, 256, 0, stream>>>(dWih, dWhh, Wattn, Wout, Wvoc, wsb);
+  k_dec<<<128, 1024, 0, stream>>>(C_idx, E_idx, C_pad, db, Wh, Wc,
+                                  pgc, pgi, pgh, pgcc, pgb, wsb, out);
+}
```

New measurement: 63.31 ms. 85.6% more time.
